# Performance work log

Hardware: AMD Instinct MI355X
Metric: run time of the kernel (lower is better)

The kernel has to match this reference:

```python
import jax, jax.numpy as jnp
import numpy as np

N_NODES = 50000
N0, N1 = 30000, 20000
N_EDGES = 600000
NUM_EDGE_TYPES = 8
NUM_NODE_TYPES = 2
IN_C, HID_C, OUT_C = 128, 128, 40


def setup_inputs() -> dict:
    key = jax.random.key(0)
    ks = jax.random.split(key, 12)
    s = 1.0 / np.sqrt(IN_C)
    inp = {
        'x0': jax.random.normal(ks[0], (N0, IN_C), jnp.float32),
        'emb1': jax.random.normal(ks[1], (N1, IN_C), jnp.float32),
        'rel_w1': jax.random.uniform(ks[2], (NUM_EDGE_TYPES, HID_C, IN_C), jnp.float32, -s, s),
        'root_w1': jax.random.uniform(ks[3], (NUM_NODE_TYPES, HID_C, IN_C), jnp.float32, -s, s),
        'root_b1': jax.random.uniform(ks[4], (NUM_NODE_TYPES, HID_C), jnp.float32, -s, s),
        'rel_w2': jax.random.uniform(ks[5], (NUM_EDGE_TYPES, OUT_C, HID_C), jnp.float32, -s, s),
        'root_w2': jax.random.uniform(ks[6], (NUM_NODE_TYPES, OUT_C, HID_C), jnp.float32, -s, s),
        'root_b2': jax.random.uniform(ks[7], (NUM_NODE_TYPES, OUT_C), jnp.float32, -s, s),
        'edge_index': jax.random.randint(ks[8], (2, N_EDGES), 0, N_NODES, jnp.int32),
        'edge_type': jax.random.randint(ks[9], (N_EDGES,), 0, NUM_EDGE_TYPES, jnp.int32),
        # nodes are ordered by type: first N0 of type 0 (featured), then N1 of type 1 (embedded)
        'node_type': jnp.concatenate([jnp.zeros(N0, jnp.int32), jnp.ones(N1, jnp.int32)]),
        'local_node_idx': jnp.concatenate([jnp.arange(N0, dtype=jnp.int32), jnp.arange(N1, dtype=jnp.int32)]),
    }
    return inp


def _group_input(x0, emb1, node_type, local_node_idx):
    mask0 = (node_type == 0)[:, None]
    h0 = x0[jnp.clip(local_node_idx, 0, N0 - 1)]
    h1 = emb1[jnp.clip(local_node_idx, 0, N1 - 1)]
    return jnp.where(mask0, h0, h1)  # [N, IN_C]


def _rgcn_conv(x, edge_index, edge_type, node_type, rel_w, root_w, root_b):
    N = x.shape[0]
    src, dst = edge_index[0], edge_index[1]
    # per-relation transform of all nodes: [T, N, out]
    x_trans = jnp.einsum('nd,tod->tno', x, rel_w)
    msg = x_trans[edge_type, src]  # [E, out] gather by (relation, source)
    # scatter-MEAN per edge type: count edges per (type, dst) segment
    comb = edge_type * N + dst
    cnt = jax.ops.segment_sum(jnp.ones_like(edge_type, dtype=x.dtype), comb,
                              num_segments=NUM_EDGE_TYPES * N)
    denom = jnp.maximum(cnt[comb], 1.0)[:, None]
    out = jax.ops.segment_sum(msg / denom, dst, num_segments=N)
    # masked per-node-type root linears
    for i in range(NUM_NODE_TYPES):
        mask = (node_type == i)[:, None]
        out = out + mask * (x @ root_w[i].T + root_b[i])
    return out


def reference(x0, emb1, rel_w1, root_w1, root_b1, rel_w2, root_w2, root_b2,
              edge_index, edge_type, node_type, local_node_idx):
    x = _group_input(x0, emb1, node_type, local_node_idx)
    x = _rgcn_conv(x, edge_index, edge_type, node_type, rel_w1, root_w1, root_b1)
    x = jax.nn.relu(x)  # dropout identity in eval mode
    x = _rgcn_conv(x, edge_index, edge_type, node_type, rel_w2, root_w2, root_b2)
    return jax.nn.log_softmax(x, axis=-1)
```

## Files before the change

kernel.cpp:

```cpp
#include <hip/hip_runtime.h>

#define NN 50000
#define NN0 30000
#define NN1 20000
#define NE 600000
#define INC 128
#define HIDC 128
#define OUTC 40
#define RSB 2304
#define KST 36
#define CAP 64
#define OVCAP 65536
#define XB 3125
#define FB 2344
#define PB 198

typedef __attribute__((ext_vector_type(4))) float f32x4;
typedef __attribute__((ext_vector_type(8))) short s16x8;

static __device__ __forceinline__ unsigned short f2bf(float f){
  unsigned u = __builtin_bit_cast(unsigned, f);
  u = u + 0x7fffu + ((u >> 16) & 1u);
  return (unsigned short)(u >> 16);
}
static __device__ __forceinline__ float bflo(unsigned w){
  return __builtin_bit_cast(float, w << 16);
}
static __device__ __forceinline__ float bfhi(unsigned w){
  return __builtin_bit_cast(float, w & 0xffff0000u);
}
static __device__ __forceinline__ void gll16(const void* g, void* l){
  __builtin_amdgcn_global_load_lds(
    (const __attribute__((address_space(1))) unsigned int*)g,
    (__attribute__((address_space(3))) unsigned int*)l, 16, 0, 0);
}

__global__ void build_k(const float* __restrict__ x0, const float* __restrict__ e1,
                        const int* __restrict__ ntp, const int* __restrict__ lix,
                        char* __restrict__ A,
                        const int* __restrict__ ei, const int* __restrict__ et,
                        int* __restrict__ deg, int* __restrict__ eb,
                        int* __restrict__ ovf, int* __restrict__ ovc,
                        const float* __restrict__ rw1, const float* __restrict__ qw1,
                        const float* __restrict__ rw2, const float* __restrict__ qw2,
                        short* __restrict__ Bp1, short* __restrict__ Bp2){
  int b = blockIdx.x;
  if(b < XB){
    int tid = b * 256 + threadIdx.x;
    int n = tid >> 4, q = tid & 15;
    if(n >= NN) return;
    int t = ntp[n], li = lix[n];
    const float* s;
    if(t == 0){ li = li < 0 ? 0 : (li > NN0 - 1 ? NN0 - 1 : li); s = x0 + (size_t)li * INC; }
    else      { li = li < 0 ? 0 : (li > NN1 - 1 ? NN1 - 1 : li); s = e1 + (size_t)li * INC; }
    float4 a = ((const float4*)s)[q * 2];
    float4 c = ((const float4*)s)[q * 2 + 1];
    uint4 o;
    o.x = (unsigned)f2bf(a.x) | ((unsigned)f2bf(a.y) << 16);
    o.y = (unsigned)f2bf(a.z) | ((unsigned)f2bf(a.w) << 16);
    o.z = (unsigned)f2bf(c.x) | ((unsigned)f2bf(c.y) << 16);
    o.w = (unsigned)f2bf(c.z) | ((unsigned)f2bf(c.w) << 16);
    *(uint4*)(A + (size_t)n * RSB + 2048 + q * 16) = o;
    return;
  }
  if(b < XB + FB){
    int e = (b - XB) * 256 + threadIdx.x;
    if(e >= NE) return;
    int s = ei[e], d = ei[NE + e], t = et[e];
    int pos = atomicAdd(&deg[d], 1);
    if(pos < CAP) eb[d * CAP + pos] = s | (t << 16);
    else { int oi = atomicAdd(ovc, 1); if(oi < OVCAP) ovf[oi] = e; }
    return;
  }
  int tid = (b - XB - FB) * 256 + threadIdx.x;
  if(tid < 2 * KST * 8 * 64){
    int l = tid & 63, j = (tid >> 6) & 7, ks = (tid >> 9) % KST, v = (tid >> 9) / KST;
    int n = j * 16 + (l & 15);
    int kb = ks * 32 + (l >> 4) * 8;
    s16x8 ov;
    #pragma unroll
    for(int jj = 0; jj < 8; jj++){
      int k = kb + jj; float wv;
      if(k < 1024){ int t = k >> 7, ki = k & 127; wv = rw1[((size_t)t * HIDC + n) * INC + ki]; }
      else        { wv = qw1[((size_t)v * HIDC + n) * INC + (k - 1024)]; }
      ov[jj] = (short)f2bf(wv);
    }
    ((s16x8*)Bp1)[tid] = ov;
    return;
  }
  int tid2 = tid - 2 * KST * 8 * 64;
  if(tid2 >= 2 * KST * 3 * 64) return;
  int l = tid2 & 63;
  int q = tid2 >> 6;
  int j = q % 3; q /= 3;
  int ks = q % KST, v = q / KST;
  int n = j * 16 + (l & 15);
  int kb = ks * 32 + (l >> 4) * 8;
  s16x8 ov;
  #pragma unroll
  for(int jj = 0; jj < 8; jj++){
    int k = kb + jj; float wv = 0.f;
    if(n < OUTC){
      if(k < 1024){ int t = k >> 7, ki = k & 127; wv = rw2[((size_t)t * OUTC + n) * INC + ki]; }
      else        { wv = qw2[((size_t)v * OUTC + n) * INC + (k - 1024)]; }
    }
    ov[jj] = (short)f2bf(wv);
  }
  ((s16x8*)Bp2)[tid2] = ov;
}

__global__ __launch_bounds__(256) void agg_k(const int* __restrict__ eb, const int* __restrict__ deg,
                                             char* __restrict__ A,
                                             const int* __restrict__ ovf, const int* __restrict__ ovc,
                                             const int* __restrict__ ei, const int* __restrict__ et){
  int wid = (blockIdx.x * 256 + threadIdx.x) >> 6;
  int l = threadIdx.x & 63;
  if(wid >= NN) return;
  int d = __builtin_amdgcn_readfirstlane(wid);
  int dg = deg[d];
  int nb = dg < CAP ? dg : CAP;
  const char* Af = A + 2048;
  int voff = l * 4;
  float acc[16];
  #pragma unroll
  for(int j = 0; j < 16; j++) acc[j] = 0.f;
  int c0 = 0, c1 = 0, c2 = 0, c3 = 0, c4 = 0, c5 = 0, c6 = 0, c7 = 0;

#define ACCUM(T, W) { \
  float fx_ = bflo(W), fy_ = bfhi(W); \
  switch(T){ \
    case 0: acc[0]  += fx_; acc[1]  += fy_; c0++; break; \
    case 1: acc[2]  += fx_; acc[3]  += fy_; c1++; break; \
    case 2: acc[4]  += fx_; acc[5]  += fy_; c2++; break; \
    case 3: acc[6]  += fx_; acc[7]  += fy_; c3++; break; \
    case 4: acc[8]  += fx_; acc[9]  += fy_; c4++; break; \
    case 5: acc[10] += fx_; acc[11] += fy_; c5++; break; \
    case 6: acc[12] += fx_; acc[13] += fy_; c6++; break; \
    default: acc[14] += fx_; acc[15] += fy_; c7++; break; \
  } }

  int base = d * CAP;
  int i = 0;
  for(; i + 3 < nb; i += 4){
    int p0 = eb[base + i + 0];
    int p1 = eb[base + i + 1];
    int p2 = eb[base + i + 2];
    int p3 = eb[base + i + 3];
    unsigned w0 = *(const unsigned*)(Af + (size_t)(p0 & 0xffff) * RSB + voff);
    unsigned w1 = *(const unsigned*)(Af + (size_t)(p1 & 0xffff) * RSB + voff);
    unsigned w2 = *(const unsigned*)(Af + (size_t)(p2 & 0xffff) * RSB + voff);
    unsigned w3 = *(const unsigned*)(Af + (size_t)(p3 & 0xffff) * RSB + voff);
    ACCUM(p0 >> 16, w0);
    ACCUM(p1 >> 16, w1);
    ACCUM(p2 >> 16, w2);
    ACCUM(p3 >> 16, w3);
  }
  for(; i < nb; i++){
    int p0 = eb[base + i];
    unsigned w0 = *(const unsigned*)(Af + (size_t)(p0 & 0xffff) * RSB + voff);
    ACCUM(p0 >> 16, w0);
  }
  if(dg > CAP){
    int oc = *ovc; if(oc > OVCAP) oc = OVCAP;
    for(int k = 0; k < oc; k++){
      int e = ovf[k];
      if(ei[NE + e] != d) continue;
      int s = ei[e];
      int t0 = et[e];
      unsigned w0 = *(const unsigned*)(Af + (size_t)s * RSB + voff);
      ACCUM(t0, w0);
    }
  }
#undef ACCUM

#define STORE(TT, CT) { \
    float iv = 1.0f / (float)((CT) > 1 ? (CT) : 1); \
    unsigned o = (unsigned)f2bf(acc[2*(TT)] * iv) | ((unsigned)f2bf(acc[2*(TT)+1] * iv) << 16); \
    *(unsigned*)(A + (size_t)d * RSB + (TT) * 256 + voff) = o; \
  }
  STORE(0, c0); STORE(1, c1); STORE(2, c2); STORE(3, c3);
  STORE(4, c4); STORE(5, c5); STORE(6, c6); STORE(7, c7);
#undef STORE
}

__global__ __launch_bounds__(512) void gemm1_k(char* __restrict__ A, const char* __restrict__ Bp,
                                               const float* __restrict__ rb, int nb0){
  __shared__ char lds[32768];
  int b = blockIdx.x;
  int v, rowbase, rowlim;
  if(b < nb0){ v = 0; rowbase = b * 128; rowlim = NN0; }
  else       { v = 1; rowbase = NN0 + (b - nb0) * 128; rowlim = NN; }
  int t = threadIdx.x, w = t >> 6, l = t & 63;
  int wr = w >> 1, wc = w & 1, lm = l & 15, lk = l >> 4;

  int srow = rowbase + (t & 127);
  if(srow > NN - 1) srow = NN - 1;
  const char* asrc = A + (size_t)srow * RSB + (t >> 7) * 16;
  const char* bsrc = Bp + (size_t)v * 294912 + t * 16;
  char* adst = lds + t * 16;
  char* bdst = lds + 16384 + t * 16;

  f32x4 acc[2][4];
  #pragma unroll
  for(int rf = 0; rf < 2; rf++)
    #pragma unroll
    for(int cf = 0; cf < 4; cf++) acc[rf][cf] = (f32x4)(0.f);

  gll16(asrc, adst);
  gll16(bsrc, bdst);
  __syncthreads();
  int cur = 0;
  #pragma unroll 1
  for(int ks = 0; ks < KST; ks++){
    int nxt = cur ^ 1;
    if(ks + 1 < KST){
      gll16(asrc + (ks + 1) * 64, adst + nxt * 8192);
      gll16(bsrc + (size_t)(ks + 1) * 8192, bdst + nxt * 8192);
    }
    const char* ab = lds + cur * 8192;
    const char* bb = lds + 16384 + cur * 8192;
    s16x8 a0 = *(const s16x8*)(ab + (lk * 128 + wr * 32 + lm) * 16);
    s16x8 a1 = *(const s16x8*)(ab + (lk * 128 + wr * 32 + 16 + lm) * 16);
    #pragma unroll
    for(int cf = 0; cf < 4; cf++){
      s16x8 bj = *(const s16x8*)(bb + ((wc * 4 + cf) * 64 + l) * 16);
      acc[0][cf] = __builtin_amdgcn_mfma_f32_16x16x32_bf16(a0, bj, acc[0][cf], 0, 0, 0);
      acc[1][cf] = __builtin_amdgcn_mfma_f32_16x16x32_bf16(a1, bj, acc[1][cf], 0, 0, 0);
    }
    __syncthreads();
    cur = nxt;
  }
  #pragma unroll
  for(int cf = 0; cf < 4; cf++){
    int col = (wc * 4 + cf) * 16 + lm;
    float bias = rb[v * HIDC + col];
    #pragma unroll
    for(int rf = 0; rf < 2; rf++){
      #pragma unroll
      for(int r = 0; r < 4; r++){
        int row = rowbase + wr * 32 + rf * 16 + lk * 4 + r;
        if(row < rowlim){
          float hv = acc[rf][cf][r] + bias;
          hv = hv > 0.f ? hv : 0.f;
          *(unsigned short*)(A + (size_t)row * RSB + 2048 + col * 2) = f2bf(hv);
        }
      }
    }
  }
}

__global__ __launch_bounds__(512) void gemm2_k(const char* __restrict__ A, const char* __restrict__ Bp,
                                               const float* __restrict__ rb, float* __restrict__ out, int nb0){
  __shared__ char lds[22528];
  int b = blockIdx.x;
  int v, rowbase, rowlim;
  if(b < nb0){ v = 0; rowbase = b * 128; rowlim = NN0; }
  else       { v = 1; rowbase = NN0 + (b - nb0) * 128; rowlim = NN; }
  int t = threadIdx.x, w = t >> 6, l = t & 63;
  int lm = l & 15, lk = l >> 4;

  int srow = rowbase + (t & 127);
  if(srow > NN - 1) srow = NN - 1;
  const char* asrc = A + (size_t)srow * RSB + (t >> 7) * 16;
  const char* bsrc = Bp + (size_t)v * 110592 + t * 16;
  char* adst = lds + t * 16;
  char* bdst = lds + 16384 + t * 16;

  f32x4 acc[3];
  #pragma unroll
  for(int j = 0; j < 3; j++) acc[j] = (f32x4)(0.f);

  gll16(asrc, adst);
  if(w < 3) gll16(bsrc, bdst);
  __syncthreads();
  int cur = 0;
  #pragma unroll 1
  for(int ks = 0; ks < KST; ks++){
    int nxt = cur ^ 1;
    if(ks + 1 < KST){
      gll16(asrc + (ks + 1) * 64, adst + nxt * 8192);
      if(w < 3) gll16(bsrc + (size_t)(ks + 1) * 3072, bdst + nxt * 3072);
    }
    const char* ab = lds + cur * 8192;
    const char* bb = lds + 16384 + cur * 3072;
    s16x8 af = *(const s16x8*)(ab + (lk * 128 + w * 16 + lm) * 16);
    #pragma unroll
    for(int j = 0; j < 3; j++){
      s16x8 bj = *(const s16x8*)(bb + (j * 64 + l) * 16);
      acc[j] = __builtin_amdgcn_mfma_f32_16x16x32_bf16(af, bj, acc[j], 0, 0, 0);
    }
    __syncthreads();
    cur = nxt;
  }

  float vals[3][4];
  #pragma unroll
  for(int j = 0; j < 3; j++){
    int col = j * 16 + lm;
    float bias = col < OUTC ? rb[v * OUTC + col] : 0.f;
    #pragma unroll
    for(int r = 0; r < 4; r++) vals[j][r] = acc[j][r] + bias;
  }
  float mx[4], se[4];
  #pragma unroll
  for(int r = 0; r < 4; r++){
    float m = -1e30f;
    #pragma unroll
    for(int j = 0; j < 3; j++) if(j * 16 + lm < OUTC) m = fmaxf(m, vals[j][r]);
    mx[r] = m;
  }
  #pragma unroll
  for(int s = 1; s < 16; s <<= 1){
    #pragma unroll
    for(int r = 0; r < 4; r++) mx[r] = fmaxf(mx[r], __shfl_xor(mx[r], s, 64));
  }
  #pragma unroll
  for(int r = 0; r < 4; r++){
    float a = 0.f;
    #pragma unroll
    for(int j = 0; j < 3; j++) if(j * 16 + lm < OUTC) a += __expf(vals[j][r] - mx[r]);
    se[r] = a;
  }
  #pragma unroll
  for(int s = 1; s < 16; s <<= 1){
    #pragma unroll
    for(int r = 0; r < 4; r++) se[r] += __shfl_xor(se[r], s, 64);
  }
  #pragma unroll
  for(int r = 0; r < 4; r++) se[r] = logf(se[r]);
  #pragma unroll
  for(int j = 0; j < 3; j++){
    int col = j * 16 + lm;
    if(col >= OUTC) continue;
    #pragma unroll
    for(int r = 0; r < 4; r++){
      int row = rowbase + w * 16 + lk * 4 + r;
      if(row < rowlim) out[(size_t)row * OUTC + col] = vals[j][r] - mx[r] - se[r];
    }
  }
}

extern "C" void kernel_launch(void* const* d_in, const int* in_sizes, int n_in,
                              void* d_out, int out_size, void* d_ws, size_t ws_size,
                              hipStream_t stream){
  const float* x0  = (const float*)d_in[0];
  const float* e1  = (const float*)d_in[1];
  const float* rw1 = (const float*)d_in[2];
  const float* qw1 = (const float*)d_in[3];
  const float* qb1 = (const float*)d_in[4];
  const float* rw2 = (const float*)d_in[5];
  const float* qw2 = (const float*)d_in[6];
  const float* qb2 = (const float*)d_in[7];
  const int*   ei  = (const int*)d_in[8];
  const int*   et  = (const int*)d_in[9];
  const int*   ntp = (const int*)d_in[10];
  const int*   lix = (const int*)d_in[11];
  float* out = (float*)d_out;

  const size_t A_OFF   = 0;
  const size_t EB_OFF  = 115200000;
  const size_t DEG_OFF = 128000000;
  const size_t OVC_OFF = 128200000;
  const size_t OVF_OFF = 128200256;
  const size_t BP1_OFF = 128462400;
  const size_t BP2_OFF = 129052224;
  const size_t TOTAL   = 129273408;
  if(ws_size < TOTAL) return;

  char* ws = (char*)d_ws;
  char*  A   = ws + A_OFF;
  int*   eb  = (int*)(ws + EB_OFF);
  int*   deg = (int*)(ws + DEG_OFF);
  int*   ovc = (int*)(ws + OVC_OFF);
  int*   ovf = (int*)(ws + OVF_OFF);
  short* Bp1 = (short*)(ws + BP1_OFF);
  short* Bp2 = (short*)(ws + BP2_OFF);

  int nb0 = (NN0 + 127) / 128;
  int nb1 = (NN - NN0 + 127) / 128;

  hipMemsetAsync(deg, 0, 200000 + 256, stream);
  build_k<<<XB + FB + PB, 256, 0, stream>>>(x0, e1, ntp, lix, A, ei, et, deg, eb, ovf, ovc,
                                            rw1, qw1, rw2, qw2, Bp1, Bp2);
  agg_k<<<(NN * 64 + 255) / 256, 256, 0, stream>>>(eb, deg, A, ovf, ovc, ei, et);
  gemm1_k<<<nb0 + nb1, 512, 0, stream>>>(A, (const char*)Bp1, qb1, nb0);
  agg_k<<<(NN * 64 + 255) / 256, 256, 0, stream>>>(eb, deg, A, ovf, ovc, ei, et);
  gemm2_k<<<nb0 + nb1, 512, 0, stream>>>(A, (const char*)Bp2, qb2, out, nb0);
}
```

Before: 304.7 us.

## Transform-then-aggregate: per-relation GEMM first, gather transformed rows, fuse epilogues

Reorders each RGCN layer so all nodes are first multiplied by the eight relation weights and the root weight into a Y buffer. A gather/mean aggregation then reads the transformed rows per edge type and fuses bias, root term, relu (layer 1) or log_softmax (layer 2). This matches the reference formulation and shrinks the layer-2 gather from 128 to 40 channels. In exchange it adds larger intermediate writes (the 9x128 Y buffer) and leaves most lanes idle in the second aggregation.

```diff
diff --git a/kernel.cpp b/kernel.cpp
--- a/kernel.cpp
+++ b/kernel.cpp
@@ -7,13 +7,15 @@
 #define INC 128
 #define HIDC 128
 #define OUTC 40
-#define RSB 2304
-#define KST 36
+#define Y1S 2304
+#define Y2S 864
+#define XS  256
 #define CAP 64
 #define OVCAP 65536
 #define XB 3125
 #define FB 2344
-#define PB 198
+#define P1T 20480
+#define P2T 7680
 
 typedef __attribute__((ext_vector_type(4))) float f32x4;
 typedef __attribute__((ext_vector_type(8))) short s16x8;
@@ -37,7 +39,7 @@
 
 __global__ void build_k(const float* __restrict__ x0, const float* __restrict__ e1,
                         const int* __restrict__ ntp, const int* __restrict__ lix,
-                        char* __restrict__ A,
+                        char* __restrict__ Xb,
                         const int* __restrict__ ei, const int* __restrict__ et,
                         int* __restrict__ deg, int* __restrict__ eb,
                         int* __restrict__ ovf, int* __restrict__ ovc,
@@ -60,7 +62,7 @@
     o.y = (unsigned)f2bf(a.z) | ((unsigned)f2bf(a.w) << 16);
     o.z = (unsigned)f2bf(c.x) | ((unsigned)f2bf(c.y) << 16);
     o.w = (unsigned)f2bf(c.z) | ((unsigned)f2bf(c.w) << 16);
-    *(uint4*)(A + (size_t)n * RSB + 2048 + q * 16) = o;
+    *(uint4*)(Xb + (size_t)n * XS + q * 16) = o;
     return;
   }
   if(b < XB + FB){
@@ -73,53 +75,176 @@
     return;
   }
   int tid = (b - XB - FB) * 256 + threadIdx.x;
-  if(tid < 2 * KST * 8 * 64){
-    int l = tid & 63, j = (tid >> 6) & 7, ks = (tid >> 9) % KST, v = (tid >> 9) / KST;
-    int n = j * 16 + (l & 15);
-    int kb = ks * 32 + (l >> 4) * 8;
+  if(tid < P1T){
+    int l = tid & 63, jf = (tid >> 6) & 7, ks = (tid >> 9) & 3, nc = tid >> 11;
+    int cc = jf * 16 + (l & 15);
+    int k0 = ks * 32 + (l >> 4) * 8;
+    const float* src = (nc < 8) ? (rw1 + ((size_t)nc * HIDC + cc) * INC + k0)
+                                : (qw1 + ((size_t)(nc - 8) * HIDC + cc) * INC + k0);
     s16x8 ov;
     #pragma unroll
-    for(int jj = 0; jj < 8; jj++){
-      int k = kb + jj; float wv;
-      if(k < 1024){ int t = k >> 7, ki = k & 127; wv = rw1[((size_t)t * HIDC + n) * INC + ki]; }
-      else        { wv = qw1[((size_t)v * HIDC + n) * INC + (k - 1024)]; }
-      ov[jj] = (short)f2bf(wv);
-    }
+    for(int jj = 0; jj < 8; jj++) ov[jj] = (short)f2bf(src[jj]);
     ((s16x8*)Bp1)[tid] = ov;
     return;
   }
-  int tid2 = tid - 2 * KST * 8 * 64;
-  if(tid2 >= 2 * KST * 3 * 64) return;
+  int tid2 = tid - P1T;
+  if(tid2 >= P2T) return;
   int l = tid2 & 63;
   int q = tid2 >> 6;
-  int j = q % 3; q /= 3;
-  int ks = q % KST, v = q / KST;
-  int n = j * 16 + (l & 15);
-  int kb = ks * 32 + (l >> 4) * 8;
+  int jf = q % 3; q /= 3;
+  int ks = q & 3, nc = q >> 2;
+  int cc = jf * 16 + (l & 15);
+  int k0 = ks * 32 + (l >> 4) * 8;
   s16x8 ov;
   #pragma unroll
   for(int jj = 0; jj < 8; jj++){
-    int k = kb + jj; float wv = 0.f;
-    if(n < OUTC){
-      if(k < 1024){ int t = k >> 7, ki = k & 127; wv = rw2[((size_t)t * OUTC + n) * INC + ki]; }
-      else        { wv = qw2[((size_t)v * OUTC + n) * INC + (k - 1024)]; }
+    float wv = 0.f;
+    if(cc < OUTC){
+      if(nc < 8) wv = rw2[((size_t)nc * OUTC + cc) * INC + k0 + jj];
+      else       wv = qw2[((size_t)(nc - 8) * OUTC + cc) * INC + k0 + jj];
     }
     ov[jj] = (short)f2bf(wv);
   }
   ((s16x8*)Bp2)[tid2] = ov;
 }
 
-__global__ __launch_bounds__(256) void agg_k(const int* __restrict__ eb, const int* __restrict__ deg,
-                                             char* __restrict__ A,
-                                             const int* __restrict__ ovf, const int* __restrict__ ovc,
-                                             const int* __restrict__ ei, const int* __restrict__ et){
+__global__ __launch_bounds__(512) void t1_k(char* __restrict__ Y, const char* __restrict__ X,
+                                            const char* __restrict__ Bp, int nb0){
+  __shared__ char lds[65536];
+  int b = blockIdx.x;
+  int v, rowbase, rowlim;
+  if(b < nb0){ v = 0; rowbase = b * 128; rowlim = NN0; }
+  else       { v = 1; rowbase = NN0 + (b - nb0) * 128; rowlim = NN; }
+  int t = threadIdx.x, w = t >> 6, l = t & 63;
+  int rg = w >> 1, cg = w & 1, lm = l & 15, lk = l >> 4;
+  int swz = (lm & 7) << 4;
+
+  #pragma unroll
+  for(int i = 0; i < 4; i++){
+    int s = t + i * 512;
+    int row = s >> 4;
+    int boff = (s & 15) * 16;
+    int srow = rowbase + row; if(srow > NN - 1) srow = NN - 1;
+    gll16(X + (size_t)srow * XS + (boff ^ ((row & 7) << 4)), lds + s * 16);
+  }
+  #pragma unroll
+  for(int i = 0; i < 4; i++){ int s = t + i * 512; gll16(Bp + s * 16, lds + 32768 + s * 16); }
+  __syncthreads();
+
+  for(int nc = 0; nc < 9; nc++){
+    f32x4 acc[2][4];
+    #pragma unroll
+    for(int rf = 0; rf < 2; rf++)
+      #pragma unroll
+      for(int cf = 0; cf < 4; cf++) acc[rf][cf] = (f32x4)(0.f);
+    #pragma unroll
+    for(int ks = 0; ks < 4; ks++){
+      int kb = ks * 64 + lk * 16;
+      int r0 = rg * 32 + lm;
+      s16x8 a0 = *(const s16x8*)(lds + r0 * 256 + (kb ^ swz));
+      s16x8 a1 = *(const s16x8*)(lds + (r0 + 16) * 256 + (kb ^ swz));
+      #pragma unroll
+      for(int cf = 0; cf < 4; cf++){
+        s16x8 bj = *(const s16x8*)(lds + 32768 + ((ks * 8 + cg * 4 + cf) * 64 + l) * 16);
+        acc[0][cf] = __builtin_amdgcn_mfma_f32_16x16x32_bf16(a0, bj, acc[0][cf], 0, 0, 0);
+        acc[1][cf] = __builtin_amdgcn_mfma_f32_16x16x32_bf16(a1, bj, acc[1][cf], 0, 0, 0);
+      }
+    }
+    __syncthreads();
+    if(nc < 8){
+      int bnc = (nc + 1 == 8) ? (8 + v) : (nc + 1);
+      const char* bs = Bp + (size_t)bnc * 32768;
+      #pragma unroll
+      for(int i = 0; i < 4; i++){ int s = t + i * 512; gll16(bs + s * 16, lds + 32768 + s * 16); }
+    }
+    #pragma unroll
+    for(int cf = 0; cf < 4; cf++){
+      int gcol = nc * 128 + cg * 64 + cf * 16 + lm;
+      #pragma unroll
+      for(int rf = 0; rf < 2; rf++){
+        #pragma unroll
+        for(int r = 0; r < 4; r++){
+          int row = rowbase + rg * 32 + rf * 16 + lk * 4 + r;
+          if(row < rowlim)
+            *(unsigned short*)(Y + (size_t)row * Y1S + gcol * 2) = f2bf(acc[rf][cf][r]);
+        }
+      }
+    }
+    __syncthreads();
+  }
+}
+
+__global__ __launch_bounds__(512) void t2_k(char* __restrict__ Y, const char* __restrict__ X,
+                                            const char* __restrict__ Bp, int nb0){
+  __shared__ char lds[45056];
+  int b = blockIdx.x;
+  int v, rowbase, rowlim;
+  if(b < nb0){ v = 0; rowbase = b * 128; rowlim = NN0; }
+  else       { v = 1; rowbase = NN0 + (b - nb0) * 128; rowlim = NN; }
+  int t = threadIdx.x, w = t >> 6, l = t & 63;
+  int lm = l & 15, lk = l >> 4;
+  int swz = (lm & 7) << 4;
+
+  #pragma unroll
+  for(int i = 0; i < 4; i++){
+    int s = t + i * 512;
+    int row = s >> 4;
+    int boff = (s & 15) * 16;
+    int srow = rowbase + row; if(srow > NN - 1) srow = NN - 1;
+    gll16(X + (size_t)srow * XS + (boff ^ ((row & 7) << 4)), lds + s * 16);
+  }
+  gll16(Bp + t * 16, lds + 32768 + t * 16);
+  if(t < 256) gll16(Bp + (512 + t) * 16, lds + 32768 + (512 + t) * 16);
+  __syncthreads();
+
+  for(int nc = 0; nc < 9; nc++){
+    f32x4 acc[3];
+    #pragma unroll
+    for(int j = 0; j < 3; j++) acc[j] = (f32x4)(0.f);
+    #pragma unroll
+    for(int ks = 0; ks < 4; ks++){
+      int kb = ks * 64 + lk * 16;
+      int row = w * 16 + lm;
+      s16x8 af = *(const s16x8*)(lds + row * 256 + (kb ^ swz));
+      #pragma unroll
+      for(int jf = 0; jf < 3; jf++){
+        s16x8 bj = *(const s16x8*)(lds + 32768 + ((ks * 3 + jf) * 64 + l) * 16);
+        acc[jf] = __builtin_amdgcn_mfma_f32_16x16x32_bf16(af, bj, acc[jf], 0, 0, 0);
+      }
+    }
+    __syncthreads();
+    if(nc < 8){
+      int bnc = (nc + 1 == 8) ? (8 + v) : (nc + 1);
+      const char* bs = Bp + (size_t)bnc * 12288;
+      gll16(bs + t * 16, lds + 32768 + t * 16);
+      if(t < 256) gll16(bs + (512 + t) * 16, lds + 32768 + (512 + t) * 16);
+    }
+    #pragma unroll
+    for(int jf = 0; jf < 3; jf++){
+      int gcol = nc * 48 + jf * 16 + lm;
+      #pragma unroll
+      for(int r = 0; r < 4; r++){
+        int row = rowbase + w * 16 + lk * 4 + r;
+        if(row < rowlim)
+          *(unsigned short*)(Y + (size_t)row * Y2S + gcol * 2) = f2bf(acc[jf][r]);
+      }
+    }
+    __syncthreads();
+  }
+}
+
+__global__ __launch_bounds__(256) void agg1_k(const int* __restrict__ eb, const int* __restrict__ deg,
+                                              const char* __restrict__ Y, char* __restrict__ Xh,
+                                              const float* __restrict__ qb1,
+                                              const int* __restrict__ ovf, const int* __restrict__ ovc,
+                                              const int* __restrict__ ei, const int* __restrict__ et){
   int wid = (blockIdx.x * 256 + threadIdx.x) >> 6;
   int l = threadIdx.x & 63;
   if(wid >= NN) return;
   int d = __builtin_amdgcn_readfirstlane(wid);
+  int v = d >= NN0 ? 1 : 0;
   int dg = deg[d];
   int nb = dg < CAP ? dg : CAP;
-  const char* Af = A + 2048;
   int voff = l * 4;
   float acc[16];
   #pragma unroll
@@ -138,6 +263,7 @@
     case 6: acc[12] += fx_; acc[13] += fy_; c6++; break; \
     default: acc[14] += fx_; acc[15] += fy_; c7++; break; \
   } }
+#define EADDR(P) (Y + (size_t)((P) & 0xffff) * Y1S + ((((P) >> 16)) << 8) + voff)
 
   int base = d * CAP;
   int i = 0;
@@ -146,10 +272,10 @@
     int p1 = eb[base + i + 1];
     int p2 = eb[base + i + 2];
     int p3 = eb[base + i + 3];
-    unsigned w0 = *(const unsigned*)(Af + (size_t)(p0 & 0xffff) * RSB + voff);
-    unsigned w1 = *(const unsigned*)(Af + (size_t)(p1 & 0xffff) * RSB + voff);
-    unsigned w2 = *(const unsigned*)(Af + (size_t)(p2 & 0xffff) * RSB + voff);
-    unsigned w3 = *(const unsigned*)(Af + (size_t)(p3 & 0xffff) * RSB + voff);
+    unsigned w0 = *(const unsigned*)EADDR(p0);
+    unsigned w1 = *(const unsigned*)EADDR(p1);
+    unsigned w2 = *(const unsigned*)EADDR(p2);
+    unsigned w3 = *(const unsigned*)EADDR(p3);
     ACCUM(p0 >> 16, w0);
     ACCUM(p1 >> 16, w1);
     ACCUM(p2 >> 16, w2);
@@ -157,7 +283,7 @@
   }
   for(; i < nb; i++){
     int p0 = eb[base + i];
-    unsigned w0 = *(const unsigned*)(Af + (size_t)(p0 & 0xffff) * RSB + voff);
+    unsigned w0 = *(const unsigned*)EADDR(p0);
     ACCUM(p0 >> 16, w0);
   }
   if(dg > CAP){
@@ -165,178 +291,120 @@
     for(int k = 0; k < oc; k++){
       int e = ovf[k];
       if(ei[NE + e] != d) continue;
-      int s = ei[e];
-      int t0 = et[e];
-      unsigned w0 = *(const unsigned*)(Af + (size_t)s * RSB + voff);
+      int s = ei[e], t0 = et[e];
+      unsigned w0 = *(const unsigned*)(Y + (size_t)s * Y1S + t0 * 256 + voff);
       ACCUM(t0, w0);
     }
   }
+#undef EADDR
 #undef ACCUM
 
-#define STORE(TT, CT) { \
-    float iv = 1.0f / (float)((CT) > 1 ? (CT) : 1); \
-    unsigned o = (unsigned)f2bf(acc[2*(TT)] * iv) | ((unsigned)f2bf(acc[2*(TT)+1] * iv) << 16); \
-    *(unsigned*)(A + (size_t)d * RSB + (TT) * 256 + voff) = o; \
-  }
-  STORE(0, c0); STORE(1, c1); STORE(2, c2); STORE(3, c3);
-  STORE(4, c4); STORE(5, c5); STORE(6, c6); STORE(7, c7);
-#undef STORE
-}
-
-__global__ __launch_bounds__(512) void gemm1_k(char* __restrict__ A, const char* __restrict__ Bp,
-                                               const float* __restrict__ rb, int nb0){
-  __shared__ char lds[32768];
-  int b = blockIdx.x;
-  int v, rowbase, rowlim;
-  if(b < nb0){ v = 0; rowbase = b * 128; rowlim = NN0; }
-  else       { v = 1; rowbase = NN0 + (b - nb0) * 128; rowlim = NN; }
-  int t = threadIdx.x, w = t >> 6, l = t & 63;
-  int wr = w >> 1, wc = w & 1, lm = l & 15, lk = l >> 4;
-
-  int srow = rowbase + (t & 127);
-  if(srow > NN - 1) srow = NN - 1;
-  const char* asrc = A + (size_t)srow * RSB + (t >> 7) * 16;
-  const char* bsrc = Bp + (size_t)v * 294912 + t * 16;
-  char* adst = lds + t * 16;
-  char* bdst = lds + 16384 + t * 16;
-
-  f32x4 acc[2][4];
-  #pragma unroll
-  for(int rf = 0; rf < 2; rf++)
-    #pragma unroll
-    for(int cf = 0; cf < 4; cf++) acc[rf][cf] = (f32x4)(0.f);
-
-  gll16(asrc, adst);
-  gll16(bsrc, bdst);
-  __syncthreads();
-  int cur = 0;
-  #pragma unroll 1
-  for(int ks = 0; ks < KST; ks++){
-    int nxt = cur ^ 1;
-    if(ks + 1 < KST){
-      gll16(asrc + (ks + 1) * 64, adst + nxt * 8192);
-      gll16(bsrc + (size_t)(ks + 1) * 8192, bdst + nxt * 8192);
-    }
-    const char* ab = lds + cur * 8192;
-    const char* bb = lds + 16384 + cur * 8192;
-    s16x8 a0 = *(const s16x8*)(ab + (lk * 128 + wr * 32 + lm) * 16);
-    s16x8 a1 = *(const s16x8*)(ab + (lk * 128 + wr * 32 + 16 + lm) * 16);
-    #pragma unroll
-    for(int cf = 0; cf < 4; cf++){
-      s16x8 bj = *(const s16x8*)(bb + ((wc * 4 + cf) * 64 + l) * 16);
-      acc[0][cf] = __builtin_amdgcn_mfma_f32_16x16x32_bf16(a0, bj, acc[0][cf], 0, 0, 0);
-      acc[1][cf] = __builtin_amdgcn_mfma_f32_16x16x32_bf16(a1, bj, acc[1][cf], 0, 0, 0);
-    }
-    __syncthreads();
-    cur = nxt;
-  }
-  #pragma unroll
-  for(int cf = 0; cf < 4; cf++){
-    int col = (wc * 4 + cf) * 16 + lm;
-    float bias = rb[v * HIDC + col];
-    #pragma unroll
-    for(int rf = 0; rf < 2; rf++){
-      #pragma unroll
-      for(int r = 0; r < 4; r++){
-        int row = rowbase + wr * 32 + rf * 16 + lk * 4 + r;
-        if(row < rowlim){
-          float hv = acc[rf][cf][r] + bias;
-          hv = hv > 0.f ? hv : 0.f;
-          *(unsigned short*)(A + (size_t)row * RSB + 2048 + col * 2) = f2bf(hv);
-        }
-      }
-    }
-  }
-}
-
-__global__ __launch_bounds__(512) void gemm2_k(const char* __restrict__ A, const char* __restrict__ Bp,
-                                               const float* __restrict__ rb, float* __restrict__ out, int nb0){
-  __shared__ char lds[22528];
-  int b = blockIdx.x;
-  int v, rowbase, rowlim;
-  if(b < nb0){ v = 0; rowbase = b * 128; rowlim = NN0; }
-  else       { v = 1; rowbase = NN0 + (b - nb0) * 128; rowlim = NN; }
-  int t = threadIdx.x, w = t >> 6, l = t & 63;
-  int lm = l & 15, lk = l >> 4;
-
-  int srow = rowbase + (t & 127);
-  if(srow > NN - 1) srow = NN - 1;
-  const char* asrc = A + (size_t)srow * RSB + (t >> 7) * 16;
-  const char* bsrc = Bp + (size_t)v * 110592 + t * 16;
-  char* adst = lds + t * 16;
-  char* bdst = lds + 16384 + t * 16;
-
-  f32x4 acc[3];
-  #pragma unroll
-  for(int j = 0; j < 3; j++) acc[j] = (f32x4)(0.f);
-
-  gll16(asrc, adst);
-  if(w < 3) gll16(bsrc, bdst);
-  __syncthreads();
-  int cur = 0;
-  #pragma unroll 1
-  for(int ks = 0; ks < KST; ks++){
-    int nxt = cur ^ 1;
-    if(ks + 1 < KST){
-      gll16(asrc + (ks + 1) * 64, adst + nxt * 8192);
-      if(w < 3) gll16(bsrc + (size_t)(ks + 1) * 3072, bdst + nxt * 3072);
-    }
-    const char* ab = lds + cur * 8192;
-    const char* bb = lds + 16384 + cur * 3072;
-    s16x8 af = *(const s16x8*)(ab + (lk * 128 + w * 16 + lm) * 16);
-    #pragma unroll
-    for(int j = 0; j < 3; j++){
-      s16x8 bj = *(const s16x8*)(bb + (j * 64 + l) * 16);
-      acc[j] = __builtin_amdgcn_mfma_f32_16x16x32_bf16(af, bj, acc[j], 0, 0, 0);
-    }
-    __syncthreads();
-    cur = nxt;
-  }
-
-  float vals[3][4];
-  #pragma unroll
-  for(int j = 0; j < 3; j++){
-    int col = j * 16 + lm;
-    float bias = col < OUTC ? rb[v * OUTC + col] : 0.f;
-    #pragma unroll
-    for(int r = 0; r < 4; r++) vals[j][r] = acc[j][r] + bias;
-  }
-  float mx[4], se[4];
-  #pragma unroll
-  for(int r = 0; r < 4; r++){
-    float m = -1e30f;
-    #pragma unroll
-    for(int j = 0; j < 3; j++) if(j * 16 + lm < OUTC) m = fmaxf(m, vals[j][r]);
-    mx[r] = m;
-  }
-  #pragma unroll
-  for(int s = 1; s < 16; s <<= 1){
-    #pragma unroll
-    for(int r = 0; r < 4; r++) mx[r] = fmaxf(mx[r], __shfl_xor(mx[r], s, 64));
-  }
-  #pragma unroll
-  for(int r = 0; r < 4; r++){
-    float a = 0.f;
-    #pragma unroll
-    for(int j = 0; j < 3; j++) if(j * 16 + lm < OUTC) a += __expf(vals[j][r] - mx[r]);
-    se[r] = a;
-  }
-  #pragma unroll
-  for(int s = 1; s < 16; s <<= 1){
-    #pragma unroll
-    for(int r = 0; r < 4; r++) se[r] += __shfl_xor(se[r], s, 64);
-  }
-  #pragma unroll
-  for(int r = 0; r < 4; r++) se[r] = logf(se[r]);
-  #pragma unroll
-  for(int j = 0; j < 3; j++){
-    int col = j * 16 + lm;
-    if(col >= OUTC) continue;
-    #pragma unroll
-    for(int r = 0; r < 4; r++){
-      int row = rowbase + w * 16 + lk * 4 + r;
-      if(row < rowlim) out[(size_t)row * OUTC + col] = vals[j][r] - mx[r] - se[r];
-    }
+  float hx = 0.f, hy = 0.f;
+#define FOLD(TT, CT) { float iv = 1.0f / (float)((CT) > 1 ? (CT) : 1); \
+    hx = fmaf(acc[2*(TT)], iv, hx); hy = fmaf(acc[2*(TT)+1], iv, hy); }
+  FOLD(0, c0); FOLD(1, c1); FOLD(2, c2); FOLD(3, c3);
+  FOLD(4, c4); FOLD(5, c5); FOLD(6, c6); FOLD(7, c7);
+#undef FOLD
+  unsigned rw = *(const unsigned*)(Y + (size_t)d * Y1S + 2048 + voff);
+  hx += bflo(rw); hy += bfhi(rw);
+  float2 bb = *(const float2*)(qb1 + v * HIDC + 2 * l);
+  hx += bb.x; hy += bb.y;
+  hx = hx > 0.f ? hx : 0.f;
+  hy = hy > 0.f ? hy : 0.f;
+  unsigned o = (unsigned)f2bf(hx) | ((unsigned)f2bf(hy) << 16);
+  *(unsigned*)(Xh + (size_t)d * XS + voff) = o;
+}
+
+__global__ __launch_bounds__(256) void agg2_k(const int* __restrict__ eb, const int* __restrict__ deg,
+                                              const char* __restrict__ Y,
+                                              const float* __restrict__ qb2, float* __restrict__ outp,
+                                              const int* __restrict__ ovf, const int* __restrict__ ovc,
+                                              const int* __restrict__ ei, const int* __restrict__ et){
+  int wid = (blockIdx.x * 256 + threadIdx.x) >> 6;
+  int l = threadIdx.x & 63;
+  if(wid >= NN) return;
+  int d = __builtin_amdgcn_readfirstlane(wid);
+  int v = d >= NN0 ? 1 : 0;
+  int dg = deg[d];
+  int nb = dg < CAP ? dg : CAP;
+  int act = l < 24;
+  int voff = l * 4;
+  float acc[16];
+  #pragma unroll
+  for(int j = 0; j < 16; j++) acc[j] = 0.f;
+  int c0 = 0, c1 = 0, c2 = 0, c3 = 0, c4 = 0, c5 = 0, c6 = 0, c7 = 0;
+
+#define ACCUM(T, W) { \
+  float fx_ = bflo(W), fy_ = bfhi(W); \
+  switch(T){ \
+    case 0: acc[0]  += fx_; acc[1]  += fy_; c0++; break; \
+    case 1: acc[2]  += fx_; acc[3]  += fy_; c1++; break; \
+    case 2: acc[4]  += fx_; acc[5]  += fy_; c2++; break; \
+    case 3: acc[6]  += fx_; acc[7]  += fy_; c3++; break; \
+    case 4: acc[8]  += fx_; acc[9]  += fy_; c4++; break; \
+    case 5: acc[10] += fx_; acc[11] += fy_; c5++; break; \
+    case 6: acc[12] += fx_; acc[13] += fy_; c6++; break; \
+    default: acc[14] += fx_; acc[15] += fy_; c7++; break; \
+  } }
+#define ELOAD(P, W) { W = 0; if(act) W = *(const unsigned*)(Y + (size_t)((P) & 0xffff) * Y2S + ((P) >> 16) * 96 + voff); }
+
+  int base = d * CAP;
+  int i = 0;
+  for(; i + 3 < nb; i += 4){
+    int p0 = eb[base + i + 0];
+    int p1 = eb[base + i + 1];
+    int p2 = eb[base + i + 2];
+    int p3 = eb[base + i + 3];
+    unsigned w0, w1, w2, w3;
+    ELOAD(p0, w0); ELOAD(p1, w1); ELOAD(p2, w2); ELOAD(p3, w3);
+    ACCUM(p0 >> 16, w0);
+    ACCUM(p1 >> 16, w1);
+    ACCUM(p2 >> 16, w2);
+    ACCUM(p3 >> 16, w3);
+  }
+  for(; i < nb; i++){
+    int p0 = eb[base + i];
+    unsigned w0; ELOAD(p0, w0);
+    ACCUM(p0 >> 16, w0);
+  }
+  if(dg > CAP){
+    int oc = *ovc; if(oc > OVCAP) oc = OVCAP;
+    for(int k = 0; k < oc; k++){
+      int e = ovf[k];
+      if(ei[NE + e] != d) continue;
+      int s = ei[e], t0 = et[e];
+      unsigned w0 = 0;
+      if(act) w0 = *(const unsigned*)(Y + (size_t)s * Y2S + t0 * 96 + voff);
+      ACCUM(t0, w0);
+    }
+  }
+#undef ELOAD
+#undef ACCUM
+
+  float vx = 0.f, vy = 0.f;
+#define FOLD(TT, CT) { float iv = 1.0f / (float)((CT) > 1 ? (CT) : 1); \
+    vx = fmaf(acc[2*(TT)], iv, vx); vy = fmaf(acc[2*(TT)+1], iv, vy); }
+  FOLD(0, c0); FOLD(1, c1); FOLD(2, c2); FOLD(3, c3);
+  FOLD(4, c4); FOLD(5, c5); FOLD(6, c6); FOLD(7, c7);
+#undef FOLD
+  if(act){
+    unsigned rw = *(const unsigned*)(Y + (size_t)d * Y2S + 768 + voff);
+    vx += bflo(rw); vy += bfhi(rw);
+  }
+  if(l < 20){
+    float2 bb = *(const float2*)(qb2 + v * OUTC + 2 * l);
+    vx += bb.x; vy += bb.y;
+  }
+  float mm = (l < 20) ? fmaxf(vx, vy) : -1e30f;
+  #pragma unroll
+  for(int s = 1; s < 64; s <<= 1) mm = fmaxf(mm, __shfl_xor(mm, s, 64));
+  float ex = (l < 20) ? (__expf(vx - mm) + __expf(vy - mm)) : 0.f;
+  #pragma unroll
+  for(int s = 1; s < 64; s <<= 1) ex += __shfl_xor(ex, s, 64);
+  float ls = logf(ex);
+  if(l < 20){
+    float2 o; o.x = vx - mm - ls; o.y = vy - mm - ls;
+    *(float2*)(outp + (size_t)d * OUTC + 2 * l) = o;
   }
 }
 
@@ -357,18 +425,20 @@
   const int*   lix = (const int*)d_in[11];
   float* out = (float*)d_out;
 
-  const size_t A_OFF   = 0;
-  const size_t EB_OFF  = 115200000;
-  const size_t DEG_OFF = 128000000;
-  const size_t OVC_OFF = 128200000;
-  const size_t OVF_OFF = 128200256;
-  const size_t BP1_OFF = 128462400;
-  const size_t BP2_OFF = 129052224;
-  const size_t TOTAL   = 129273408;
+  const size_t Y_OFF   = 0;
+  const size_t X_OFF   = 115200000;
+  const size_t EB_OFF  = 128000000;
+  const size_t DEG_OFF = 140800000;
+  const size_t OVC_OFF = 141000000;
+  const size_t OVF_OFF = 141000256;
+  const size_t BP1_OFF = 141262400;
+  const size_t BP2_OFF = 141590080;
+  const size_t TOTAL   = 141712960;
   if(ws_size < TOTAL) return;
 
   char* ws = (char*)d_ws;
-  char*  A   = ws + A_OFF;
+  char*  Y   = ws + Y_OFF;
+  char*  X   = ws + X_OFF;
   int*   eb  = (int*)(ws + EB_OFF);
   int*   deg = (int*)(ws + DEG_OFF);
   int*   ovc = (int*)(ws + OVC_OFF);
@@ -378,12 +448,14 @@
 
   int nb0 = (NN0 + 127) / 128;
   int nb1 = (NN - NN0 + 127) / 128;
+  int p1b = P1T / 256;
+  int p2b = P2T / 256;
 
   hipMemsetAsync(deg, 0, 200000 + 256, stream);
-  build_k<<<XB + FB + PB, 256, 0, stream>>>(x0, e1, ntp, lix, A, ei, et, deg, eb, ovf, ovc,
-                                            rw1, qw1, rw2, qw2, Bp1, Bp2);
-  agg_k<<<(NN * 64 + 255) / 256, 256, 0, stream>>>(eb, deg, A, ovf, ovc, ei, et);
-  gemm1_k<<<nb0 + nb1, 512, 0, stream>>>(A, (const char*)Bp1, qb1, nb0);
-  agg_k<<<(NN * 64 + 255) / 256, 256, 0, stream>>>(eb, deg, A, ovf, ovc, ei, et);
-  gemm2_k<<<nb0 + nb1, 512, 0, stream>>>(A, (const char*)Bp2, qb2, out, nb0);
-}
+  build_k<<<XB + FB + p1b + p2b, 256, 0, stream>>>(x0, e1, ntp, lix, X, ei, et, deg, eb, ovf, ovc,
+                                                   rw1, qw1, rw2, qw2, Bp1, Bp2);
+  t1_k<<<nb0 + nb1, 512, 0, stream>>>(Y, X, (const char*)Bp1, nb0);
+  agg1_k<<<(NN + 3) / 4, 256, 0, stream>>>(eb, deg, Y, X, qb1, ovf, ovc, ei, et);
+  t2_k<<<nb0 + nb1, 512, 0, stream>>>(Y, X, (const char*)Bp2, nb0);
+  agg2_k<<<(NN + 3) / 4, 256, 0, stream>>>(eb, deg, Y, qb2, out, ovf, ovc, ei, et);
+}
```

New measurement: 295.1 us. 1.03x faster.
